# Optimization experiments

Hardware: AMD Instinct MI355X
Metric: run time of the kernel (lower is better)

## Reference

```python
import jax, jax.numpy as jnp
import numpy as np

E = 262144   # number of edges
B = 8192     # buckets per grouping
D = 32       # uniform bucket degree (B*D == E)
DIM = 128    # in_feats
OUT = 128    # out_feats


def setup_inputs() -> dict:
    key = jax.random.key(0)
    ks = jax.random.split(key, 12)
    src_feat = jax.random.normal(ks[0], (E, DIM), jnp.float32)
    dst_feat = jax.random.normal(ks[1], (E, DIM), jnp.float32)
    timestamp = jax.random.uniform(ks[2], (E,), jnp.float32) * 100.0
    # grouping permutations: flat edge order -> buckets of uniform degree
    src_perm = jax.random.permutation(ks[3], E).astype(jnp.int32)
    dst_perm = jax.random.permutation(ks[4], E).astype(jnp.int32)
    # causal deg_indices: index of most recent valid temporal neighbor, <= position
    pos = jnp.arange(D, dtype=jnp.int32)[None, :]
    src_deg_indices = jnp.minimum(jax.random.randint(ks[5], (B, D), 0, D, jnp.int32), pos)
    dst_deg_indices = jnp.minimum(jax.random.randint(ks[6], (B, D), 0, D, jnp.int32), pos)
    # TimeEncodingLayer('cosine') params
    basis_freq = 0.1 * jnp.linspace(0.0, 9.0, DIM, dtype=jnp.float32)
    phase = jnp.zeros((DIM,), jnp.float32)
    W_time = jax.random.normal(ks[7], (DIM, 2 * DIM), jnp.float32) * 0.05
    b_time = jnp.zeros((DIM,), jnp.float32)
    # fc_self / fc_neigh
    W_self = jax.random.normal(ks[8], (OUT, DIM), jnp.float32) * 0.05
    b_self = jnp.zeros((OUT,), jnp.float32)
    W_neigh = jax.random.normal(ks[9], (OUT, DIM), jnp.float32) * 0.05
    b_neigh = jnp.zeros((OUT,), jnp.float32)
    return dict(src_feat=src_feat, dst_feat=dst_feat, timestamp=timestamp,
                basis_freq=basis_freq, phase=phase, W_time=W_time, b_time=b_time,
                W_self=W_self, b_self=b_self, W_neigh=W_neigh, b_neigh=b_neigh,
                src_perm=src_perm, dst_perm=dst_perm,
                src_deg_indices=src_deg_indices, dst_deg_indices=dst_deg_indices)


def _encode_time(u, t, basis_freq, phase, W_time, b_time):
    # cosine time encoding: cos(t * freq + phase), concat with u, linear, relu
    tt = jnp.cos(t[:, None] * basis_freq[None, :] + phase[None, :])  # [E, DIM]
    x = jnp.concatenate([u, tt], axis=-1) @ W_time.T + b_time
    return jax.nn.relu(x)


def _mean_conv(h_self_e, h_neigh_e, perm, idx, W_self, b_self, W_neigh, b_neigh):
    # gather flat edge features into [B, D, DIM] buckets
    hs = h_self_e[perm].reshape(B, D, DIM)
    hn = h_neigh_e[perm].reshape(B, D, DIM)
    # mean aggregator: cumsum / (deg_indices+1), then gather at deg_indices
    mean_cof = (idx.astype(hn.dtype) + 1.0)[:, :, None]          # [B, D, 1]
    h_feat = jnp.cumsum(hn, axis=1) / mean_cof                    # [B, D, DIM]
    mask_feat = jnp.take_along_axis(h_feat, idx[:, :, None], axis=1)  # [B, D, DIM]
    rst = hs @ W_self.T + b_self + mask_feat @ W_neigh.T + b_neigh    # [B, D, OUT]
    # scatter back to flat edge order
    return jnp.zeros((E, OUT), rst.dtype).at[perm].set(rst.reshape(E, OUT))


def reference(src_feat, dst_feat, timestamp, basis_freq, phase, W_time, b_time,
              W_self, b_self, W_neigh, b_neigh,
              src_perm, dst_perm, src_deg_indices, dst_deg_indices):
    enc_src = _encode_time(src_feat, timestamp, basis_freq, phase, W_time, b_time)
    enc_dst = _encode_time(dst_feat, timestamp, basis_freq, phase, W_time, b_time)
    # groupby='src': self = src embedding, neighbors = dst embeddings
    src_out = _mean_conv(enc_src, enc_dst, src_perm, src_deg_indices,
                         W_self, b_self, W_neigh, b_neigh)
    # groupby='dst': self = dst embedding, neighbors = src embeddings
    dst_out = _mean_conv(enc_dst, enc_src, dst_perm, dst_deg_indices,
                         W_self, b_self, W_neigh, b_neigh)
    return src_out, dst_out
```

## Files before the change

kernel.cpp:

```cpp
#include <hip/hip_runtime.h>
#include <hip/hip_bf16.h>
#include <math.h>

#define E_EDGES 262144
#define NBUCKET 8192
#define DEG     32
#define FDIM    128

typedef float f32x4 __attribute__((ext_vector_type(4)));
typedef short s16x8 __attribute__((ext_vector_type(8)));
typedef short s16x4 __attribute__((ext_vector_type(4)));

typedef const __attribute__((address_space(1))) unsigned g_u32;
typedef __attribute__((address_space(3))) unsigned l_u32;

__device__ __forceinline__ short f2bf(float f) {
    __hip_bfloat16 h = __float2bfloat16(f);
    return *reinterpret_cast<short*>(&h);
}
__device__ __forceinline__ float bf2f(short s) {
    union { unsigned u; float f; } v; v.u = ((unsigned)(unsigned short)s) << 16;
    return v.f;
}

__device__ __forceinline__ s16x8 read_wfrag(const short* w_lds, int n, int k0) {
    int byte = ((n << 8) + (k0 << 1)) ^ ((n & 7) << 4);
    return *reinterpret_cast<const s16x8*>(reinterpret_cast<const char*>(w_lds) + byte);
}

__device__ __forceinline__ void stage_w(short* w_lds, const float* __restrict__ Wg,
                                        int stride, int tid) {
    #pragma unroll
    for (int it = 0; it < 16; ++it) {
        int i  = it * 256 + tid;
        int n  = i >> 5;
        int k4 = (i & 31) << 2;
        const float4 v = *reinterpret_cast<const float4*>(Wg + (size_t)n * stride + k4);
        s16x4 h; h[0]=f2bf(v.x); h[1]=f2bf(v.y); h[2]=f2bf(v.z); h[3]=f2bf(v.w);
        int byte = ((n << 8) + (k4 << 1)) ^ ((n & 7) << 4);
        *reinterpret_cast<s16x4*>(reinterpret_cast<char*>(w_lds) + byte) = h;
    }
}

__device__ __forceinline__ void dma_w32k(const short* __restrict__ gsw, short* lds, int tid) {
    const int lane = tid & 63, wid = tid >> 6;
    const char* g = reinterpret_cast<const char*>(gsw);
    char* l = reinterpret_cast<char*>(lds);
    #pragma unroll
    for (int i = 0; i < 8; ++i) {
        const int off = i * 4096 + wid * 1024;
        __builtin_amdgcn_global_load_lds((g_u32*)(g + off + lane * 16),
                                         (l_u32*)(l + off), 16, 0, 0);
    }
}

__global__ void prep_kernel(const float* __restrict__ W_time,
                            const float* __restrict__ W_self,
                            const float* __restrict__ W_neigh,
                            short* __restrict__ Wswz)
{
    const int t = blockIdx.x * 256 + threadIdx.x;
    const int region = t >> 11;
    const int chunk  = t & 2047;
    const int n = chunk >> 4;
    const int c = chunk & 15;

    const float* src;
    if      (region == 0) src = W_time  + n * 256 + c * 8;
    else if (region == 1) src = W_time  + n * 256 + 128 + c * 8;
    else if (region == 2) src = W_self  + n * 128 + c * 8;
    else                  src = W_neigh + n * 128 + c * 8;

    const float4 lo = *reinterpret_cast<const float4*>(src);
    const float4 hi = *reinterpret_cast<const float4*>(src + 4);
    s16x8 h;
    h[0]=f2bf(lo.x); h[1]=f2bf(lo.y); h[2]=f2bf(lo.z); h[3]=f2bf(lo.w);
    h[4]=f2bf(hi.x); h[5]=f2bf(hi.y); h[6]=f2bf(hi.z); h[7]=f2bf(hi.w);

    const int byte = (region << 15) + ((((n << 8) + (c << 4)) ^ ((n & 7) << 4)));
    *reinterpret_cast<s16x8*>(reinterpret_cast<char*>(Wswz) + byte) = h;
}

__global__ __launch_bounds__(512, 4)
void encode_kernel(const float* __restrict__ src_feat,
                   const float* __restrict__ dst_feat,
                   const float* __restrict__ ts,
                   const float* __restrict__ freq,
                   const float* __restrict__ ph,
                   const short* __restrict__ Wswz,
                   const float* __restrict__ b_time,
                   short* __restrict__ enc_src,
                   short* __restrict__ enc_dst)
{
    __shared__ short w_lds[2][128 * 128];

    const int tid  = threadIdx.x;
    const int lane = tid & 63;
    const int wid  = tid >> 6;
    const int lrow = lane & 15;
    const int klo  = (lane >> 4) << 3;
    const int r0   = blockIdx.x * 128 + wid * 16;

    float4 sf[8], df[8];
    #pragma unroll
    for (int kb = 0; kb < 4; ++kb) {
        const float* ps = src_feat + (size_t)(r0 + lrow) * FDIM + kb * 32 + klo;
        const float* pd = dst_feat + (size_t)(r0 + lrow) * FDIM + kb * 32 + klo;
        sf[kb*2]   = *reinterpret_cast<const float4*>(ps);
        sf[kb*2+1] = *reinterpret_cast<const float4*>(ps + 4);
        df[kb*2]   = *reinterpret_cast<const float4*>(pd);
        df[kb*2+1] = *reinterpret_cast<const float4*>(pd + 4);
    }

    {
        const char* g = reinterpret_cast<const char*>(Wswz);
        char* l = reinterpret_cast<char*>(&w_lds[0][0]);
        #pragma unroll
        for (int i = 0; i < 8; ++i) {
            const int off = i * 8192 + wid * 1024;
            __builtin_amdgcn_global_load_lds((g_u32*)(g + off + lane * 16),
                                             (l_u32*)(l + off), 16, 0, 0);
        }
    }

    const float t_row = ts[r0 + lrow];
    s16x8 tf[4];
    #pragma unroll
    for (int kb = 0; kb < 4; ++kb) {
        s16x8 t;
        #pragma unroll
        for (int j = 0; j < 8; ++j) {
            const int k = kb * 32 + klo + j;
            t[j] = f2bf(__cosf(fmaf(t_row, freq[k], ph[k])));
        }
        tf[kb] = t;
    }

    s16x8 as_[4], ad_[4];
    #pragma unroll
    for (int kb = 0; kb < 4; ++kb) {
        s16x8 a, b;
        #pragma unroll
        for (int j = 0; j < 4; ++j) {
            a[j]   = f2bf(sf[kb*2][j]);   a[4+j] = f2bf(sf[kb*2+1][j]);
            b[j]   = f2bf(df[kb*2][j]);   b[4+j] = f2bf(df[kb*2+1][j]);
        }
        as_[kb] = a; ad_[kb] = b;
    }
    __syncthreads();

    const int rbase = r0 + ((lane >> 4) << 2);
    #pragma unroll
    for (int nt = 0; nt < 8; ++nt) {
        const int n = nt * 16 + lrow;
        f32x4 a = {0.f, 0.f, 0.f, 0.f};
        #pragma unroll
        for (int kb = 0; kb < 4; ++kb)
            a = __builtin_amdgcn_mfma_f32_16x16x32_bf16(
                    tf[kb], read_wfrag(w_lds[1], n, kb * 32 + klo), a, 0, 0, 0);
        f32x4 b = a;
        #pragma unroll
        for (int kb = 0; kb < 4; ++kb) {
            const s16x8 wf = read_wfrag(w_lds[0], n, kb * 32 + klo);
            a = __builtin_amdgcn_mfma_f32_16x16x32_bf16(as_[kb], wf, a, 0, 0, 0);
            b = __builtin_amdgcn_mfma_f32_16x16x32_bf16(ad_[kb], wf, b, 0, 0, 0);
        }
        const int col = nt * 16 + lrow;
        const float bias = b_time[col];
        #pragma unroll
        for (int r = 0; r < 4; ++r) {
            float es = a[r] + bias; es = es > 0.f ? es : 0.f;
            float ed = b[r] + bias; ed = ed > 0.f ? ed : 0.f;
            enc_src[(size_t)(rbase + r) * FDIM + col] = f2bf(es);
            enc_dst[(size_t)(rbase + r) * FDIM + col] = f2bf(ed);
        }
    }
}

__global__ __launch_bounds__(256, 2)
void encode_fallback(const float* __restrict__ src_feat,
                     const float* __restrict__ dst_feat,
                     const float* __restrict__ ts,
                     const float* __restrict__ freq,
                     const float* __restrict__ ph,
                     const float* __restrict__ W_time,
                     const float* __restrict__ b_time,
                     short* __restrict__ enc_src,
                     short* __restrict__ enc_dst)
{
    __shared__ short w_lds[128 * 128];
    const int tid  = threadIdx.x;
    const int lane = tid & 63;
    const int wid  = tid >> 6;
    const int r0   = blockIdx.x * 64 + wid * 16;
    const int lrow = lane & 15;
    const int klo  = (lane >> 4) << 3;

    stage_w(w_lds, W_time + 128, 256, tid);
    const float t_row = ts[r0 + lrow];
    s16x8 tf[4];
    #pragma unroll
    for (int kb = 0; kb < 4; ++kb) {
        const int k = kb * 32 + klo;
        s16x8 t;
        #pragma unroll
        for (int j = 0; j < 8; ++j)
            t[j] = f2bf(__cosf(fmaf(t_row, freq[k + j], ph[k + j])));
        tf[kb] = t;
    }
    __syncthreads();
    f32x4 S[8];
    #pragma unroll
    for (int nt = 0; nt < 8; ++nt) {
        f32x4 a = {0.f, 0.f, 0.f, 0.f};
        #pragma unroll
        for (int kb = 0; kb < 4; ++kb)
            a = __builtin_amdgcn_mfma_f32_16x16x32_bf16(
                    tf[kb], read_wfrag(w_lds, nt * 16 + lrow, kb * 32 + klo), a, 0, 0, 0);
        S[nt] = a;
    }
    __syncthreads();
    stage_w(w_lds, W_time, 256, tid);
    __syncthreads();
    #pragma unroll
    for (int s = 0; s < 2; ++s) {
        const float* feat = s ? dst_feat : src_feat;
        short*       enc  = s ? enc_dst  : enc_src;
        s16x8 af[4];
        #pragma unroll
        for (int kb = 0; kb < 4; ++kb) {
            const float* p = feat + (size_t)(r0 + lrow) * FDIM + kb * 32 + klo;
            const float4 lo = *reinterpret_cast<const float4*>(p);
            const float4 hi = *reinterpret_cast<const float4*>(p + 4);
            s16x8 a;
            a[0]=f2bf(lo.x); a[1]=f2bf(lo.y); a[2]=f2bf(lo.z); a[3]=f2bf(lo.w);
            a[4]=f2bf(hi.x); a[5]=f2bf(hi.y); a[6]=f2bf(hi.z); a[7]=f2bf(hi.w);
            af[kb] = a;
        }
        #pragma unroll
        for (int nt = 0; nt < 8; ++nt) {
            f32x4 acc = S[nt];
            #pragma unroll
            for (int kb = 0; kb < 4; ++kb)
                acc = __builtin_amdgcn_mfma_f32_16x16x32_bf16(
                        af[kb], read_wfrag(w_lds, nt * 16 + lrow, kb * 32 + klo), acc, 0, 0, 0);
            const int col  = nt * 16 + lrow;
            const float bias = b_time[col];
            const int rbase = r0 + ((lane >> 4) << 2);
            #pragma unroll
            for (int r = 0; r < 4; ++r) {
                float e = acc[r] + bias;
                e = e > 0.f ? e : 0.f;
                enc[(size_t)(rbase + r) * FDIM + col] = f2bf(e);
            }
        }
    }
}

template<int DMA>
__global__ __launch_bounds__(256, 3)
void conv_kernel(const short* __restrict__ enc_src,
                 const short* __restrict__ enc_dst,
                 const short* __restrict__ Wswz_self,
                 const short* __restrict__ Wswz_neigh,
                 const float* __restrict__ W_self,
                 const float* __restrict__ W_neigh,
                 const float* __restrict__ b_self,
                 const float* __restrict__ b_neigh,
                 const int* __restrict__ src_perm,
                 const int* __restrict__ dst_perm,
                 const int* __restrict__ src_idx,
                 const int* __restrict__ dst_idx,
                 float* __restrict__ out)
{
    __shared__ short w_lds[128 * 128];
    __shared__ short hf[2][DEG * 128];
    __shared__ int   perm_s[2][DEG];
    __shared__ int   idx_s[2][DEG];
    __shared__ float bias_s[128];

    const int tid = threadIdx.x;
    const int g   = blockIdx.y;
    const int b0  = blockIdx.x * 2;

    const short* enc_self  = g ? enc_dst : enc_src;
    const short* enc_neigh = g ? enc_src : enc_dst;
    const int*   perm      = g ? dst_perm : src_perm;
    const int*   degi      = g ? dst_idx  : src_idx;
    float*       outg      = out + (size_t)g * E_EDGES * FDIM;

    if (DMA) dma_w32k(Wswz_self, w_lds, tid);

    if (tid < 64) {
        const int lb = tid >> 5, d = tid & 31;
        perm_s[lb][d] = perm[(b0 + lb) * DEG + d];
        idx_s[lb][d]  = degi[(b0 + lb) * DEG + d];
    } else if (tid < 192) {
        const int c = tid - 64;
        bias_s[c] = b_self[c] + b_neigh[c];
    }
    if (!DMA) stage_w(w_lds, W_self, 128, tid);
    __syncthreads();

    const int lane = tid & 63;
    const int wid  = tid >> 6;
    const int lb   = wid >> 1;
    const int mt   = wid & 1;
    const int lrow = lane & 15;
    const int klo  = (lane >> 4) << 3;
    const int row  = mt * 16 + lrow;

    s16x8 hsf[4];
    {
        const int e = perm_s[lb][row];
        const short* p = enc_self + (size_t)e * FDIM;
        #pragma unroll
        for (int kb = 0; kb < 4; ++kb)
            hsf[kb] = *reinterpret_cast<const s16x8*>(p + kb * 32 + klo);
    }

    const int lbc = tid >> 7;
    const int c   = tid & 127;
    unsigned short cum[DEG];
    #pragma unroll
    for (int d = 0; d < DEG; ++d) {
        const int e = perm_s[lbc][d];
        cum[d] = *reinterpret_cast<const unsigned short*>(
                     enc_neigh + (size_t)e * FDIM + c);
    }

    f32x4 acc[8];
    #pragma unroll
    for (int nt = 0; nt < 8; ++nt) {
        f32x4 a = {0.f, 0.f, 0.f, 0.f};
        #pragma unroll
        for (int kb = 0; kb < 4; ++kb)
            a = __builtin_amdgcn_mfma_f32_16x16x32_bf16(
                    hsf[kb], read_wfrag(w_lds, nt * 16 + lrow, kb * 32 + klo), a, 0, 0, 0);
        acc[nt] = a;
    }

    {
        float run = 0.f;
        #pragma unroll
        for (int d = 0; d < DEG; ++d) {
            run += bf2f((short)cum[d]);
            const float inv = __builtin_amdgcn_rcpf((float)(idx_s[lbc][d] + 1));
            const int byte = ((d << 8) + (c << 1)) ^ ((d & 7) << 4);
            *reinterpret_cast<short*>(reinterpret_cast<char*>(hf[lbc]) + byte)
                = f2bf(run * inv);
        }
    }

    __syncthreads();
    if (DMA) dma_w32k(Wswz_neigh, w_lds, tid);
    else     stage_w(w_lds, W_neigh, 128, tid);
    __syncthreads();

    s16x8 mff[4];
    {
        const int j = idx_s[lb][row];
        #pragma unroll
        for (int kb = 0; kb < 4; ++kb) {
            const int byte = ((j << 8) + ((kb * 32 + klo) << 1)) ^ ((j & 7) << 4);
            mff[kb] = *reinterpret_cast<const s16x8*>(
                          reinterpret_cast<const char*>(hf[lb]) + byte);
        }
    }
    #pragma unroll
    for (int nt = 0; nt < 8; ++nt) {
        f32x4 a = acc[nt];
        #pragma unroll
        for (int kb = 0; kb < 4; ++kb)
            a = __builtin_amdgcn_mfma_f32_16x16x32_bf16(
                    mff[kb], read_wfrag(w_lds, nt * 16 + lrow, kb * 32 + klo), a, 0, 0, 0);
        acc[nt] = a;
    }

    __syncthreads();
    {
        float* epl = reinterpret_cast<float*>(w_lds) + wid * 2048;
        #pragma unroll
        for (int nt = 0; nt < 8; ++nt) {
            const int col = nt * 16 + lrow;
            const float bias = bias_s[col];
            #pragma unroll
            for (int r = 0; r < 4; ++r) {
                const int rtile = ((lane >> 4) << 2) + r;
                epl[rtile * 128 + col] = acc[nt][r] + bias;
            }
        }
        asm volatile("s_waitcnt lgkmcnt(0)" ::: "memory");
        __builtin_amdgcn_sched_barrier(0);
        #pragma unroll
        for (int i = 0; i < 8; ++i) {
            const int rtile = i * 2 + (lane >> 5);
            const int c4    = (lane & 31) * 4;
            const f32x4 v = *reinterpret_cast<const f32x4*>(epl + rtile * 128 + c4);
            const int e = perm_s[lb][mt * 16 + rtile];
            *reinterpret_cast<f32x4*>(outg + (size_t)e * FDIM + c4) = v;
        }
    }
}

extern "C" void kernel_launch(void* const* d_in, const int* in_sizes, int n_in,
                              void* d_out, int out_size, void* d_ws, size_t ws_size,
                              hipStream_t stream) {
    (void)in_sizes; (void)n_in; (void)out_size;

    const float* src_feat = (const float*)d_in[0];
    const float* dst_feat = (const float*)d_in[1];
    const float* ts       = (const float*)d_in[2];
    const float* freq     = (const float*)d_in[3];
    const float* ph       = (const float*)d_in[4];
    const float* W_time   = (const float*)d_in[5];
    const float* b_time   = (const float*)d_in[6];
    const float* W_self   = (const float*)d_in[7];
    const float* b_self   = (const float*)d_in[8];
    const float* W_neigh  = (const float*)d_in[9];
    const float* b_neigh  = (const float*)d_in[10];
    const int*   src_perm = (const int*)d_in[11];
    const int*   dst_perm = (const int*)d_in[12];
    const int*   src_idx  = (const int*)d_in[13];
    const int*   dst_idx  = (const int*)d_in[14];

    short* enc_src = (short*)d_ws;
    short* enc_dst = enc_src + (size_t)E_EDGES * FDIM;
    short* Wswz    = enc_dst + (size_t)E_EDGES * FDIM;
    const size_t need = (size_t)E_EDGES * FDIM * 2 * 2 + 4 * 32768;

    if (ws_size >= need) {
        prep_kernel<<<dim3(32), dim3(256), 0, stream>>>(W_time, W_self, W_neigh, Wswz);
        encode_kernel<<<dim3(E_EDGES / 128), dim3(512), 0, stream>>>(
            src_feat, dst_feat, ts, freq, ph, Wswz, b_time, enc_src, enc_dst);
        conv_kernel<1><<<dim3(NBUCKET / 2, 2), dim3(256), 0, stream>>>(
            enc_src, enc_dst, Wswz + 2 * 16384, Wswz + 3 * 16384, W_self, W_neigh,
            b_self, b_neigh, src_perm, dst_perm, src_idx, dst_idx, (float*)d_out);
    } else {
        encode_fallback<<<dim3(E_EDGES / 64), dim3(256), 0, stream>>>(
            src_feat, dst_feat, ts, freq, ph, W_time, b_time, enc_src, enc_dst);
        conv_kernel<0><<<dim3(NBUCKET / 2, 2), dim3(256), 0, stream>>>(
            enc_src, enc_dst, (const short*)nullptr, (const short*)nullptr,
            W_self, W_neigh, b_self, b_neigh,
            src_perm, dst_perm, src_idx, dst_idx, (float*)d_out);
    }
}
```

Measured before the change: 239.7 us.

## Swap MFMA operands for row-contiguous vector stores and split cumsum work

Swaps the A/B operands of the MFMA calls so each lane's accumulator holds four consecutive output channels of one row. The encode and conv epilogues can then write packed 8-byte bf16 or 16-byte fp32 vectors straight to global memory, which removes the LDS transpose staging and its barrier in conv. The neighbour cumsum now runs on two waves that each load packed bf16 pairs, instead of all four waves loading single shorts. The summed bias is precomputed in prep_kernel, at the cost of leaving two waves idle during the cumsum and adding a small extra workspace requirement.

```diff
diff --git a/kernel.cpp b/kernel.cpp
--- a/kernel.cpp
+++ b/kernel.cpp
@@ -57,28 +57,36 @@
 __global__ void prep_kernel(const float* __restrict__ W_time,
                             const float* __restrict__ W_self,
                             const float* __restrict__ W_neigh,
-                            short* __restrict__ Wswz)
+                            const float* __restrict__ b_self,
+                            const float* __restrict__ b_neigh,
+                            short* __restrict__ Wswz,
+                            float* __restrict__ bsum)
 {
     const int t = blockIdx.x * 256 + threadIdx.x;
-    const int region = t >> 11;
-    const int chunk  = t & 2047;
-    const int n = chunk >> 4;
-    const int c = chunk & 15;
-
-    const float* src;
-    if      (region == 0) src = W_time  + n * 256 + c * 8;
-    else if (region == 1) src = W_time  + n * 256 + 128 + c * 8;
-    else if (region == 2) src = W_self  + n * 128 + c * 8;
-    else                  src = W_neigh + n * 128 + c * 8;
-
-    const float4 lo = *reinterpret_cast<const float4*>(src);
-    const float4 hi = *reinterpret_cast<const float4*>(src + 4);
-    s16x8 h;
-    h[0]=f2bf(lo.x); h[1]=f2bf(lo.y); h[2]=f2bf(lo.z); h[3]=f2bf(lo.w);
-    h[4]=f2bf(hi.x); h[5]=f2bf(hi.y); h[6]=f2bf(hi.z); h[7]=f2bf(hi.w);
-
-    const int byte = (region << 15) + ((((n << 8) + (c << 4)) ^ ((n & 7) << 4)));
-    *reinterpret_cast<s16x8*>(reinterpret_cast<char*>(Wswz) + byte) = h;
+    if (t < 8192) {
+        const int region = t >> 11;
+        const int chunk  = t & 2047;
+        const int n = chunk >> 4;
+        const int c = chunk & 15;
+
+        const float* src;
+        if      (region == 0) src = W_time  + n * 256 + c * 8;
+        else if (region == 1) src = W_time  + n * 256 + 128 + c * 8;
+        else if (region == 2) src = W_self  + n * 128 + c * 8;
+        else                  src = W_neigh + n * 128 + c * 8;
+
+        const float4 lo = *reinterpret_cast<const float4*>(src);
+        const float4 hi = *reinterpret_cast<const float4*>(src + 4);
+        s16x8 h;
+        h[0]=f2bf(lo.x); h[1]=f2bf(lo.y); h[2]=f2bf(lo.z); h[3]=f2bf(lo.w);
+        h[4]=f2bf(hi.x); h[5]=f2bf(hi.y); h[6]=f2bf(hi.z); h[7]=f2bf(hi.w);
+
+        const int byte = (region << 15) + ((((n << 8) + (c << 4)) ^ ((n & 7) << 4)));
+        *reinterpret_cast<s16x8*>(reinterpret_cast<char*>(Wswz) + byte) = h;
+    } else if (t < 8192 + 128) {
+        const int c = t - 8192;
+        bsum[c] = b_self[c] + b_neigh[c];
+    }
 }
 
 __global__ __launch_bounds__(512, 4)
@@ -98,7 +106,8 @@
     const int lane = tid & 63;
     const int wid  = tid >> 6;
     const int lrow = lane & 15;
-    const int klo  = (lane >> 4) << 3;
+    const int q    = lane >> 4;
+    const int klo  = q << 3;
     const int r0   = blockIdx.x * 128 + wid * 16;
 
     float4 sf[8], df[8];
@@ -149,7 +158,6 @@
     }
     __syncthreads();
 
-    const int rbase = r0 + ((lane >> 4) << 2);
     #pragma unroll
     for (int nt = 0; nt < 8; ++nt) {
         const int n = nt * 16 + lrow;
@@ -157,23 +165,25 @@
         #pragma unroll
         for (int kb = 0; kb < 4; ++kb)
             a = __builtin_amdgcn_mfma_f32_16x16x32_bf16(
-                    tf[kb], read_wfrag(w_lds[1], n, kb * 32 + klo), a, 0, 0, 0);
+                    read_wfrag(w_lds[1], n, kb * 32 + klo), tf[kb], a, 0, 0, 0);
         f32x4 b = a;
         #pragma unroll
         for (int kb = 0; kb < 4; ++kb) {
             const s16x8 wf = read_wfrag(w_lds[0], n, kb * 32 + klo);
-            a = __builtin_amdgcn_mfma_f32_16x16x32_bf16(as_[kb], wf, a, 0, 0, 0);
-            b = __builtin_amdgcn_mfma_f32_16x16x32_bf16(ad_[kb], wf, b, 0, 0, 0);
-        }
-        const int col = nt * 16 + lrow;
-        const float bias = b_time[col];
+            a = __builtin_amdgcn_mfma_f32_16x16x32_bf16(wf, as_[kb], a, 0, 0, 0);
+            b = __builtin_amdgcn_mfma_f32_16x16x32_bf16(wf, ad_[kb], b, 0, 0, 0);
+        }
+        const int ch = nt * 16 + q * 4;
+        const float4 bias4 = *reinterpret_cast<const float4*>(b_time + ch);
+        s16x4 ss, sd;
         #pragma unroll
         for (int r = 0; r < 4; ++r) {
-            float es = a[r] + bias; es = es > 0.f ? es : 0.f;
-            float ed = b[r] + bias; ed = ed > 0.f ? ed : 0.f;
-            enc_src[(size_t)(rbase + r) * FDIM + col] = f2bf(es);
-            enc_dst[(size_t)(rbase + r) * FDIM + col] = f2bf(ed);
-        }
+            float es = a[r] + bias4[r]; es = es > 0.f ? es : 0.f;
+            float ed = b[r] + bias4[r]; ed = ed > 0.f ? ed : 0.f;
+            ss[r] = f2bf(es); sd[r] = f2bf(ed);
+        }
+        *reinterpret_cast<s16x4*>(enc_src + (size_t)(r0 + lrow) * FDIM + ch) = ss;
+        *reinterpret_cast<s16x4*>(enc_dst + (size_t)(r0 + lrow) * FDIM + ch) = sd;
     }
 }
 
@@ -265,6 +275,7 @@
                  const short* __restrict__ Wswz_neigh,
                  const float* __restrict__ W_self,
                  const float* __restrict__ W_neigh,
+                 const float* __restrict__ bsum,
                  const float* __restrict__ b_self,
                  const float* __restrict__ b_neigh,
                  const int* __restrict__ src_perm,
@@ -277,7 +288,6 @@
     __shared__ short hf[2][DEG * 128];
     __shared__ int   perm_s[2][DEG];
     __shared__ int   idx_s[2][DEG];
-    __shared__ float bias_s[128];
 
     const int tid = threadIdx.x;
     const int g   = blockIdx.y;
@@ -295,9 +305,6 @@
         const int lb = tid >> 5, d = tid & 31;
         perm_s[lb][d] = perm[(b0 + lb) * DEG + d];
         idx_s[lb][d]  = degi[(b0 + lb) * DEG + d];
-    } else if (tid < 192) {
-        const int c = tid - 64;
-        bias_s[c] = b_self[c] + b_neigh[c];
     }
     if (!DMA) stage_w(w_lds, W_self, 128, tid);
     __syncthreads();
@@ -307,7 +314,8 @@
     const int lb   = wid >> 1;
     const int mt   = wid & 1;
     const int lrow = lane & 15;
-    const int klo  = (lane >> 4) << 3;
+    const int q    = lane >> 4;
+    const int klo  = q << 3;
     const int row  = mt * 16 + lrow;
 
     s16x8 hsf[4];
@@ -319,14 +327,14 @@
             hsf[kb] = *reinterpret_cast<const s16x8*>(p + kb * 32 + klo);
     }
 
-    const int lbc = tid >> 7;
-    const int c   = tid & 127;
-    unsigned short cum[DEG];
-    #pragma unroll
-    for (int d = 0; d < DEG; ++d) {
-        const int e = perm_s[lbc][d];
-        cum[d] = *reinterpret_cast<const unsigned short*>(
-                     enc_neigh + (size_t)e * FDIM + c);
+    unsigned cum[DEG];
+    if (wid < 2) {
+        #pragma unroll
+        for (int d = 0; d < DEG; ++d) {
+            const int e = perm_s[wid][d];
+            cum[d] = *reinterpret_cast<const unsigned*>(
+                         enc_neigh + (size_t)e * FDIM + 2 * lane);
+        }
     }
 
     f32x4 acc[8];
@@ -336,19 +344,21 @@
         #pragma unroll
         for (int kb = 0; kb < 4; ++kb)
             a = __builtin_amdgcn_mfma_f32_16x16x32_bf16(
-                    hsf[kb], read_wfrag(w_lds, nt * 16 + lrow, kb * 32 + klo), a, 0, 0, 0);
+                    read_wfrag(w_lds, nt * 16 + lrow, kb * 32 + klo), hsf[kb], a, 0, 0, 0);
         acc[nt] = a;
     }
 
-    {
-        float run = 0.f;
+    if (wid < 2) {
+        float run0 = 0.f, run1 = 0.f;
         #pragma unroll
         for (int d = 0; d < DEG; ++d) {
-            run += bf2f((short)cum[d]);
-            const float inv = __builtin_amdgcn_rcpf((float)(idx_s[lbc][d] + 1));
-            const int byte = ((d << 8) + (c << 1)) ^ ((d & 7) << 4);
-            *reinterpret_cast<short*>(reinterpret_cast<char*>(hf[lbc]) + byte)
-                = f2bf(run * inv);
+            run0 += bf2f((short)(cum[d] & 0xFFFFu));
+            run1 += bf2f((short)(cum[d] >> 16));
+            const float inv = __builtin_amdgcn_rcpf((float)(idx_s[wid][d] + 1));
+            const unsigned pk = (unsigned)(unsigned short)f2bf(run0 * inv)
+                              | ((unsigned)(unsigned short)f2bf(run1 * inv) << 16);
+            const int byte = ((d << 8) + (lane << 2)) ^ ((d & 7) << 4);
+            *reinterpret_cast<unsigned*>(reinterpret_cast<char*>(hf[wid]) + byte) = pk;
         }
     }
 
@@ -373,32 +383,27 @@
         #pragma unroll
         for (int kb = 0; kb < 4; ++kb)
             a = __builtin_amdgcn_mfma_f32_16x16x32_bf16(
-                    mff[kb], read_wfrag(w_lds, nt * 16 + lrow, kb * 32 + klo), a, 0, 0, 0);
+                    read_wfrag(w_lds, nt * 16 + lrow, kb * 32 + klo), mff[kb], a, 0, 0, 0);
         acc[nt] = a;
     }
 
-    __syncthreads();
     {
-        float* epl = reinterpret_cast<float*>(w_lds) + wid * 2048;
+        const int e = perm_s[lb][row];
+        float* po = outg + (size_t)e * FDIM;
         #pragma unroll
         for (int nt = 0; nt < 8; ++nt) {
-            const int col = nt * 16 + lrow;
-            const float bias = bias_s[col];
-            #pragma unroll
-            for (int r = 0; r < 4; ++r) {
-                const int rtile = ((lane >> 4) << 2) + r;
-                epl[rtile * 128 + col] = acc[nt][r] + bias;
+            const int ch = nt * 16 + q * 4;
+            float4 bs4;
+            if (DMA) bs4 = *reinterpret_cast<const float4*>(bsum + ch);
+            else {
+                const float4 s4 = *reinterpret_cast<const float4*>(b_self + ch);
+                const float4 n4 = *reinterpret_cast<const float4*>(b_neigh + ch);
+                bs4 = make_float4(s4.x+n4.x, s4.y+n4.y, s4.z+n4.z, s4.w+n4.w);
             }
-        }
-        asm volatile("s_waitcnt lgkmcnt(0)" ::: "memory");
-        __builtin_amdgcn_sched_barrier(0);
-        #pragma unroll
-        for (int i = 0; i < 8; ++i) {
-            const int rtile = i * 2 + (lane >> 5);
-            const int c4    = (lane & 31) * 4;
-            const f32x4 v = *reinterpret_cast<const f32x4*>(epl + rtile * 128 + c4);
-            const int e = perm_s[lb][mt * 16 + rtile];
-            *reinterpret_cast<f32x4*>(outg + (size_t)e * FDIM + c4) = v;
+            f32x4 v;
+            v[0] = acc[nt][0] + bs4.x; v[1] = acc[nt][1] + bs4.y;
+            v[2] = acc[nt][2] + bs4.z; v[3] = acc[nt][3] + bs4.w;
+            *reinterpret_cast<f32x4*>(po + ch) = v;
         }
     }
 }
@@ -427,21 +432,23 @@
     short* enc_src = (short*)d_ws;
     short* enc_dst = enc_src + (size_t)E_EDGES * FDIM;
     short* Wswz    = enc_dst + (size_t)E_EDGES * FDIM;
-    const size_t need = (size_t)E_EDGES * FDIM * 2 * 2 + 4 * 32768;
+    float* bsum    = (float*)(Wswz + 4 * 16384);
+    const size_t need = (size_t)E_EDGES * FDIM * 2 * 2 + 4 * 32768 + 512;
 
     if (ws_size >= need) {
-        prep_kernel<<<dim3(32), dim3(256), 0, stream>>>(W_time, W_self, W_neigh, Wswz);
+        prep_kernel<<<dim3(33), dim3(256), 0, stream>>>(
+            W_time, W_self, W_neigh, b_self, b_neigh, Wswz, bsum);
         encode_kernel<<<dim3(E_EDGES / 128), dim3(512), 0, stream>>>(
             src_feat, dst_feat, ts, freq, ph, Wswz, b_time, enc_src, enc_dst);
         conv_kernel<1><<<dim3(NBUCKET / 2, 2), dim3(256), 0, stream>>>(
             enc_src, enc_dst, Wswz + 2 * 16384, Wswz + 3 * 16384, W_self, W_neigh,
-            b_self, b_neigh, src_perm, dst_perm, src_idx, dst_idx, (float*)d_out);
+            bsum, b_self, b_neigh, src_perm, dst_perm, src_idx, dst_idx, (float*)d_out);
     } else {
         encode_fallback<<<dim3(E_EDGES / 64), dim3(256), 0, stream>>>(
             src_feat, dst_feat, ts, freq, ph, W_time, b_time, enc_src, enc_dst);
         conv_kernel<0><<<dim3(NBUCKET / 2, 2), dim3(256), 0, stream>>>(
             enc_src, enc_dst, (const short*)nullptr, (const short*)nullptr,
-            W_self, W_neigh, b_self, b_neigh,
+            W_self, W_neigh, (const float*)nullptr, b_self, b_neigh,
             src_perm, dst_perm, src_idx, dst_idx, (float*)d_out);
     }
 }
```

Measured after the change: 254.2 us. +6.1%, slower.
